# Kernel tuning notes

Measured on AMD Instinct MI355X. Metric: run time of the kernel, lower is better.

Reference implementation:

```python
import jax, jax.numpy as jnp
import numpy as np

D_MODEL = 1024
NHEAD = 16
SPARSITY = 0.9  # keep prob = 1 - sparsity
NEG = -1e30    # stand-in for -inf; avoids NaN on (rare) fully-masked rows
EPS = 1e-5


def _layernorm(x, g, b):
    mu = jnp.mean(x, axis=-1, keepdims=True)
    var = jnp.mean(jnp.square(x - mu), axis=-1, keepdims=True)
    return (x - mu) * jax.lax.rsqrt(var + EPS) * g + b


def setup_inputs() -> dict:
    key = jax.random.key(0)
    ks = jax.random.split(key, 12)
    B, S, D = 2, 2048, D_MODEL
    H = NHEAD
    s = 1.0 / np.sqrt(D)
    inp = {
        "x": jax.random.normal(ks[0], (B, S, D), jnp.float32),
        # torch: torch.rand((B,H,S,S)) > sparsity, resampled each forward
        "mask": jax.random.uniform(ks[1], (B, H, S, S), jnp.float32) > SPARSITY,
        "Wq": jax.random.normal(ks[2], (D, D), jnp.float32) * s,
        "bq": jnp.zeros((D,), jnp.float32),
        "Wk": jax.random.normal(ks[3], (D, D), jnp.float32) * s,
        "bk": jnp.zeros((D,), jnp.float32),
        "Wv": jax.random.normal(ks[4], (D, D), jnp.float32) * s,
        "bv": jnp.zeros((D,), jnp.float32),
        "Wo": jax.random.normal(ks[5], (D, D), jnp.float32) * s,
        "bo": jnp.zeros((D,), jnp.float32),
        "ln1_g": jnp.ones((D,), jnp.float32),
        "ln1_b": jnp.zeros((D,), jnp.float32),
        "ln2_g": jnp.ones((D,), jnp.float32),
        "ln2_b": jnp.zeros((D,), jnp.float32),
        "W1": jax.random.normal(ks[6], (D, 4 * D), jnp.float32) * s,
        "b1f": jnp.zeros((4 * D,), jnp.float32),
        "W2": jax.random.normal(ks[7], (4 * D, D), jnp.float32) * (1.0 / np.sqrt(4 * D)),
        "b2f": jnp.zeros((D,), jnp.float32),
    }
    return inp


def reference(x, mask, Wq, bq, Wk, bk, Wv, bv, Wo, bo,
              ln1_g, ln1_b, ln2_g, ln2_b, W1, b1f, W2, b2f):
    B, S, D = x.shape
    H = NHEAD
    dk = D // H
    # projections -> (B, H, S, dk)
    q = (x @ Wq + bq).reshape(B, S, H, dk).transpose(0, 2, 1, 3)
    k = (x @ Wk + bk).reshape(B, S, H, dk).transpose(0, 2, 1, 3)
    v = (x @ Wv + bv).reshape(B, S, H, dk).transpose(0, 2, 1, 3)
    scores = jnp.einsum('bhqd,bhkd->bhqk', q, k) / np.sqrt(dk)
    scores = jnp.where(mask, scores, NEG)
    attn = jax.nn.softmax(scores, axis=-1)
    ctx = jnp.einsum('bhqk,bhkd->bhqd', attn, v)          # (B,H,S,dk)
    ctx = ctx.transpose(0, 2, 1, 3).reshape(B, S, D)
    attn_out = ctx @ Wo + bo
    x = _layernorm(x + attn_out, ln1_g, ln1_b)
    ff = jax.nn.relu(x @ W1 + b1f) @ W2 + b2f             # eval: dropout off
    return _layernorm(x + ff, ln2_g, ln2_b)
```

## Files before the change

kernel.cpp:

```cpp
#include <hip/hip_runtime.h>
#include <stdint.h>


typedef __attribute__((ext_vector_type(8))) short short8;
typedef __attribute__((ext_vector_type(4))) float f32x4;
typedef __attribute__((ext_vector_type(4))) unsigned short u16x4;

__device__ __forceinline__ unsigned short f2bf(float f) {
    union { float f; unsigned u; } v; v.f = f;
    unsigned r = v.u + 0x7fffu + ((v.u >> 16) & 1u);
    return (unsigned short)(r >> 16);
}

__device__ __forceinline__ void gload16(const void* gsrc, void* ldst) {
    __builtin_amdgcn_global_load_lds(
        (const __attribute__((address_space(1))) void*)gsrc,
        (__attribute__((address_space(3))) void*)ldst,
        16, 0, 0);
}

__device__ __forceinline__ int SWZ(int b) { return b ^ (((b >> 9) & 1) << 5); }

__global__ __launch_bounds__(256) void f32_to_bf16_k(
    const float* __restrict__ in, unsigned short* __restrict__ out, int n4)
{
    int i = blockIdx.x * 256 + threadIdx.x;
    if (i < n4) {
        f32x4 v = *(const f32x4*)&in[(size_t)i * 4];
        u16x4 o = { f2bf(v[0]), f2bf(v[1]), f2bf(v[2]), f2bf(v[3]) };
        *(u16x4*)&out[(size_t)i * 4] = o;
    }
}

__global__ __launch_bounds__(256) void transpose_k(
    const float* __restrict__ W, unsigned short* __restrict__ Wt, int K, int N)
{
    __shared__ float tile[32][33];
    const int n0 = blockIdx.x * 32, k0 = blockIdx.y * 32;
    const int tx = threadIdx.x & 31, ty = threadIdx.x >> 5;
#pragma unroll
    for (int i = 0; i < 32; i += 8)
        tile[ty + i][tx] = W[(size_t)(k0 + ty + i) * N + n0 + tx];
    __syncthreads();
#pragma unroll
    for (int i = 0; i < 32; i += 8)
        Wt[(size_t)(n0 + ty + i) * K + k0 + tx] = f2bf(tile[tx][ty + i]);
}

__global__ __launch_bounds__(256) void vtrans_k(
    const unsigned short* __restrict__ qkv, unsigned short* __restrict__ vt)
{
    __shared__ unsigned short tile[32][34];
    const int s0 = blockIdx.x * 32;
    const int d0 = blockIdx.y * 32;
    const int bh = blockIdx.z, b = bh >> 4, h = bh & 15;
    const int tx = threadIdx.x & 31, ty = threadIdx.x >> 5;
#pragma unroll
    for (int i = 0; i < 32; i += 8)
        tile[ty + i][tx] = qkv[(size_t)(b * 2048 + s0 + ty + i) * 3072 + 2048 + h * 64 + d0 + tx];
    __syncthreads();
#pragma unroll
    for (int i = 0; i < 32; i += 8)
        vt[((size_t)bh * 64 + d0 + ty + i) * 2048 + s0 + tx] = tile[tx][ty + i];
}

__global__ void concat3_k(const float* a, const float* b, const float* c, float* out)
{
    int i = blockIdx.x * 256 + threadIdx.x;
    if (i < 3072) out[i] = (i < 1024) ? a[i] : (i < 2048 ? b[i - 1024] : c[i - 2048]);
}

__global__ __launch_bounds__(1024) void detect_mask_k(
    const unsigned int* __restrict__ m, int* __restrict__ flag)
{
    __shared__ int f1, f2;
    if (threadIdx.x == 0) { f1 = 0; f2 = 0; }
    __syncthreads();
    int l1 = 0, l2 = 0;
    for (int i = threadIdx.x; i < 65536; i += 1024) {
        unsigned v = m[i];
        l1 |= (v > 1u);
        l2 |= (v != 0u && v != 0x3f800000u);
    }
    if (l1) atomicOr(&f1, 1);
    if (l2) atomicOr(&f2, 1);
    __syncthreads();
    if (threadIdx.x == 0) {
        int mode = 0;
        if (f1) mode = f2 ? 1 : 2;
        *flag = mode;
    }
}

__global__ __launch_bounds__(256) void pack_mask_k(
    const void* __restrict__ mask, const int* __restrict__ flag,
    unsigned long long* __restrict__ packed, long long nelem)
{
    const int mode = *flag;
    const long long stride = (long long)gridDim.x * 256;
    long long i = (long long)blockIdx.x * 256 + threadIdx.x;
    if (mode == 0) {
        const int* m = (const int*)mask;
        for (; i < nelem; i += stride) {
            unsigned long long bl = __ballot(m[i] != 0);
            if ((threadIdx.x & 63) == 0) packed[i >> 6] = bl;
        }
    } else if (mode == 1) {
        const unsigned char* m = (const unsigned char*)mask;
        for (; i < nelem; i += stride) {
            unsigned long long bl = __ballot(m[i] != 0);
            if ((threadIdx.x & 63) == 0) packed[i >> 6] = bl;
        }
    } else {
        const float* m = (const float*)mask;
        for (; i < nelem; i += stride) {
            unsigned long long bl = __ballot(m[i] != 0.f);
            if ((threadIdx.x & 63) == 0) packed[i >> 6] = bl;
        }
    }
}

template<int EPI>
__global__ __launch_bounds__(512) void gemm256_bt(
    const unsigned short* __restrict__ A, const unsigned short* __restrict__ Bt,
    const float* __restrict__ bias, void* __restrict__ Cout,
    int M, int N, int K)
{
    __shared__ __align__(16) unsigned short lds[2][2][256 * 64];
    const int t = threadIdx.x;
    const int lane = t & 63;
    const int wid = t >> 6;
    const int l16 = lane & 15, g = lane >> 4;
    const int wr = wid >> 2, wc = wid & 3;

    const int nbx = gridDim.x, nwg = nbx * gridDim.y;
    const int orig = blockIdx.y * nbx + blockIdx.x;
    const int qq = nwg >> 3, rr = nwg & 7;
    const int xcd = orig & 7, idx = orig >> 3;
    const int wg = (xcd < rr) ? (xcd * (qq + 1) + idx)
                              : (rr * (qq + 1) + (xcd - rr) * qq + idx);
    const int bm = (wg / nbx) * 256, bn = (wg % nbx) * 256;

    const int ntiles = K >> 6;
    auto kof = [&](int s) { return (s < ntiles ? s : ntiles - 1) << 6; };

    auto stage_half = [&](const unsigned short* __restrict__ P, int grow0, int k0,
                          int buf, int ab, int half) {
#pragma unroll
        for (int rnd = 0; rnd < 2; ++rnd) {
            const int off = rnd * 8192 + t * 16;
            const int sw  = SWZ(off);
            const int row = off >> 7;
            const int col = (sw & 127) >> 1;
            gload16(&P[(size_t)(grow0 + half * 128 + row) * K + k0 + col],
                    &lds[buf][ab][half * 8192 + (off >> 1)]);
        }
    };

    auto lda = [&](int buf, int m, int kc) -> short8 {
        const int byte = ((m * 32 + wr * 16 + l16) * 64 + kc * 32 + g * 8) * 2;
        return *(const short8*)((const char*)&lds[buf][0][0] + SWZ(byte));
    };
    auto ldb = [&](int buf, int n, int kc) -> short8 {
        const int byte = ((n * 64 + wc * 16 + l16) * 64 + kc * 32 + g * 8) * 2;
        return *(const short8*)((const char*)&lds[buf][1][0] + SWZ(byte));
    };

    f32x4 acc[8][4] = {};
    short8 af[4][2];

    stage_half(A,  bm, 0,  0, 0, 0);
    stage_half(A,  bm, 0,  0, 0, 1);
    stage_half(Bt, bn, 0,  0, 1, 0);
    stage_half(Bt, bn, 0,  0, 1, 1);
    stage_half(A,  bm, 64, 1, 0, 0);
    stage_half(Bt, bn, 64, 1, 1, 0);
    asm volatile("s_waitcnt vmcnt(4)" ::: "memory");
    __builtin_amdgcn_s_barrier();

#define PH(buf, mh, nh, doLoadA, STAGE_STMT, doVM)                                  \
  {                                                                                  \
    if (doLoadA) {                                                                   \
      _Pragma("unroll") for (int mm = 0; mm < 4; ++mm)                               \
      _Pragma("unroll") for (int kc = 0; kc < 2; ++kc)                               \
        af[mm][kc] = lda(buf, (mh) * 4 + mm, kc);                                    \
    }                                                                                \
    short8 bf[2][2];                                                                 \
    _Pragma("unroll") for (int nn = 0; nn < 2; ++nn)                                 \
    _Pragma("unroll") for (int kc = 0; kc < 2; ++kc)                                 \
      bf[nn][kc] = ldb(buf, (nh) * 2 + nn, kc);                                      \
    STAGE_STMT;                                                                      \
    __builtin_amdgcn_s_barrier();                                                    \
    __builtin_amdgcn_s_setprio(1);                                                   \
    _Pragma("unroll") for (int mm = 0; mm < 4; ++mm)                                 \
    _Pragma("unroll") for (int nn = 0; nn < 2; ++nn)                                 \
    _Pragma("unroll") for (int kc = 0; kc < 2; ++kc)                                 \
      acc[(mh) * 4 + mm][(nh) * 2 + nn] = __builtin_amdgcn_mfma_f32_16x16x32_bf16(   \
          af[mm][kc], bf[nn][kc], acc[(mh) * 4 + mm][(nh) * 2 + nn], 0, 0, 0);       \
    __builtin_amdgcn_s_setprio(0);                                                   \
    if (doVM) { asm volatile("s_waitcnt vmcnt(4)" ::: "memory"); }                   \
    __builtin_amdgcn_s_barrier();                                                    \
  }

    const int half_ntiles = ntiles >> 1;
    for (int i = 0; i < half_ntiles; ++i) {
        const int k1 = (2 * i + 1) << 6;
        const int k2 = kof(2 * i + 2);
        const int k3 = kof(2 * i + 3);
        PH(0, 0, 0, 1, (stage_half(A,  bm, k1, 1, 0, 1)), 0)
        PH(0, 0, 1, 0, (stage_half(Bt, bn, k1, 1, 1, 1)), 0)
        PH(0, 1, 0, 1, (stage_half(A,  bm, k2, 0, 0, 0)), 0)
        PH(0, 1, 1, 0, (stage_half(Bt, bn, k2, 0, 1, 0)), 1)
        PH(1, 0, 0, 1, (stage_half(A,  bm, k2, 0, 0, 1)), 0)
        PH(1, 0, 1, 0, (stage_half(Bt, bn, k2, 0, 1, 1)), 0)
        PH(1, 1, 0, 1, (stage_half(A,  bm, k3, 1, 0, 0)), 0)
        PH(1, 1, 1, 0, (stage_half(Bt, bn, k3, 1, 1, 0)), 1)
    }
#undef PH

#pragma unroll
    for (int m = 0; m < 8; ++m) {
        const int row0 = bm + m * 32 + wr * 16 + g * 4;
#pragma unroll
        for (int n = 0; n < 4; ++n) {
            const int col = bn + n * 64 + wc * 16 + l16;
            const float bb = bias[col];
#pragma unroll
            for (int r = 0; r < 4; ++r) {
                float v = acc[m][n][r] + bb;
                if (EPI == 1) v = fmaxf(v, 0.f);
                ((unsigned short*)Cout)[(size_t)(row0 + r) * N + col] = f2bf(v);
            }
        }
    }
}

template<int EPI>
__global__ __launch_bounds__(256) void gemm_bt(
    const unsigned short* __restrict__ A, const unsigned short* __restrict__ Bt,
    const float* __restrict__ bias, const float* __restrict__ resid,
    void* __restrict__ Cout, int M, int N, int K)
{
    __shared__ unsigned short As[128 * 64];
    __shared__ unsigned short Bs[128 * 64];
    const int t = threadIdx.x;
    const int lane = t & 63, wid = t >> 6;
    const int l16 = lane & 15, g = lane >> 4;
    const int wr = wid >> 1, wc = wid & 1;
    const int bm = blockIdx.y * 128, bn = blockIdx.x * 128;

    f32x4 acc[4][4] = {};

    for (int k0 = 0; k0 < K; k0 += 64) {
        __syncthreads();
#pragma unroll
        for (int i = 0; i < 4; ++i) {
            int linear = i * 2048 + t * 8;
            int row = linear >> 6, col = linear & 63;
            gload16(&A[(size_t)(bm + row) * K + k0 + col], &As[linear]);
        }
#pragma unroll
        for (int i = 0; i < 4; ++i) {
            int linear = i * 2048 + t * 8;
            int row = linear >> 6, col = linear & 63;
            gload16(&Bt[(size_t)(bn + row) * K + k0 + col], &Bs[linear]);
        }
        __syncthreads();
#pragma unroll
        for (int kc = 0; kc < 2; ++kc) {
            short8 a[4], b[4];
#pragma unroll
            for (int m = 0; m < 4; ++m)
                a[m] = *(const short8*)&As[(wr * 64 + m * 16 + l16) * 64 + kc * 32 + g * 8];
#pragma unroll
            for (int n = 0; n < 4; ++n)
                b[n] = *(const short8*)&Bs[(wc * 64 + n * 16 + l16) * 64 + kc * 32 + g * 8];
#pragma unroll
            for (int m = 0; m < 4; ++m)
#pragma unroll
                for (int n = 0; n < 4; ++n)
                    acc[m][n] = __builtin_amdgcn_mfma_f32_16x16x32_bf16(a[m], b[n], acc[m][n], 0, 0, 0);
        }
    }

#pragma unroll
    for (int m = 0; m < 4; ++m) {
        const int row0 = bm + wr * 64 + m * 16 + g * 4;
#pragma unroll
        for (int n = 0; n < 4; ++n) {
            const int col = bn + wc * 64 + n * 16 + l16;
            const float bb = bias[col];
#pragma unroll
            for (int r = 0; r < 4; ++r) {
                float v = acc[m][n][r] + bb;
                const size_t idx = (size_t)(row0 + r) * N + col;
                if (EPI == 2) {
                    ((float*)Cout)[idx] = v + resid[idx];
                } else {
                    if (EPI == 1) v = fmaxf(v, 0.f);
                    ((unsigned short*)Cout)[idx] = f2bf(v);
                }
            }
        }
    }
}

__global__ __launch_bounds__(256) void attn_k(
    const unsigned short* __restrict__ qkv,
    const unsigned short* __restrict__ vt,
    const unsigned long long* __restrict__ pmask,
    unsigned short* __restrict__ ctx)
{
    __shared__ unsigned short Pl[4][16 * 72];
    const int t = threadIdx.x, lane = t & 63, w = t >> 6;
    const int l16 = lane & 15, g = lane >> 4;
    const int bh = blockIdx.y;
    const int b = bh >> 4, h = bh & 15;
    const int q0 = blockIdx.x * 64;

    const size_t rowQ = (size_t)(b * 2048 + q0 + w * 16 + l16) * 3072 + h * 64;
    const short8 qf0 = *(const short8*)&qkv[rowQ + g * 8];
    const short8 qf1 = *(const short8*)&qkv[rowQ + 32 + g * 8];

    const unsigned long long* mbase =
        pmask + ((size_t)bh * 2048 + q0 + w * 16 + g * 4) * 32;
    const unsigned short* vbase = &vt[(size_t)bh * 64 * 2048];

    f32x4 acc[4] = {};
    float mrow[4], lrow[4];
#pragma unroll
    for (int j = 0; j < 4; ++j) { mrow[j] = -INFINITY; lrow[j] = 0.f; }

    for (int kt = 0; kt < 32; ++kt) {
        unsigned long long mw[4];
#pragma unroll
        for (int j = 0; j < 4; ++j) mw[j] = mbase[j * 32 + kt];

        f32x4 s[4] = {};
#pragma unroll
        for (int n = 0; n < 4; ++n) {
            const size_t rowK = (size_t)(b * 2048 + kt * 64 + n * 16 + l16) * 3072 + 1024 + h * 64;
            const short8 kf0 = *(const short8*)&qkv[rowK + g * 8];
            const short8 kf1 = *(const short8*)&qkv[rowK + 32 + g * 8];
            s[n] = __builtin_amdgcn_mfma_f32_16x16x32_bf16(qf0, kf0, s[n], 0, 0, 0);
            s[n] = __builtin_amdgcn_mfma_f32_16x16x32_bf16(qf1, kf1, s[n], 0, 0, 0);
        }

#pragma unroll
        for (int n = 0; n < 4; ++n) {
            const int sh = n * 16 + l16;
#pragma unroll
            for (int j = 0; j < 4; ++j) {
                const bool keep = (mw[j] >> sh) & 1ull;
                s[n][j] = keep ? s[n][j] * 0.125f : -1e30f;
            }
        }

#pragma unroll
        for (int j = 0; j < 4; ++j) {
            float mx = fmaxf(fmaxf(s[0][j], s[1][j]), fmaxf(s[2][j], s[3][j]));
#pragma unroll
            for (int d = 1; d < 16; d <<= 1) mx = fmaxf(mx, __shfl_xor(mx, d));
            const float mn = fmaxf(mrow[j], mx);
            float p0 = __expf(s[0][j] - mn), p1 = __expf(s[1][j] - mn);
            float p2 = __expf(s[2][j] - mn), p3 = __expf(s[3][j] - mn);
            s[0][j] = p0; s[1][j] = p1; s[2][j] = p2; s[3][j] = p3;
            float sm = p0 + p1 + p2 + p3;
#pragma unroll
            for (int d = 1; d < 16; d <<= 1) sm += __shfl_xor(sm, d);
            const float scale = __expf(mrow[j] - mn);
            lrow[j] = lrow[j] * scale + sm;
            mrow[j] = mn;
#pragma unroll
            for (int n = 0; n < 4; ++n) acc[n][j] *= scale;
        }

#pragma unroll
        for (int n = 0; n < 4; ++n)
#pragma unroll
            for (int j = 0; j < 4; ++j)
                Pl[w][(g * 4 + j) * 72 + n * 16 + l16] = f2bf(s[n][j]);

#pragma unroll
        for (int c = 0; c < 2; ++c) {
            const short8 pf = *(const short8*)&Pl[w][l16 * 72 + c * 32 + g * 8];
#pragma unroll
            for (int n = 0; n < 4; ++n) {
                const short8 vf = *(const short8*)&vbase[(size_t)(n * 16 + l16) * 2048 + kt * 64 + c * 32 + g * 8];
                acc[n] = __builtin_amdgcn_mfma_f32_16x16x32_bf16(pf, vf, acc[n], 0, 0, 0);
            }
        }
    }

#pragma unroll
    for (int n = 0; n < 4; ++n)
#pragma unroll
        for (int j = 0; j < 4; ++j) {
            const int q = q0 + w * 16 + g * 4 + j;
            ctx[(size_t)(b * 2048 + q) * 1024 + h * 64 + n * 16 + l16] = f2bf(acc[n][j] / lrow[j]);
        }
}

template<int WB>
__global__ __launch_bounds__(256) void ln_k(
    const float* __restrict__ in, const float* __restrict__ gw, const float* __restrict__ bw,
    float* __restrict__ outF, unsigned short* __restrict__ outB)
{
    __shared__ float red[2][4];
    const int row = blockIdx.x, t = threadIdx.x;
    const f32x4 v = *(const f32x4*)&in[(size_t)row * 1024 + t * 4];
    float s = v[0] + v[1] + v[2] + v[3];
    float ss = v[0] * v[0] + v[1] * v[1] + v[2] * v[2] + v[3] * v[3];
#pragma unroll
    for (int d = 1; d < 64; d <<= 1) { s += __shfl_xor(s, d); ss += __shfl_xor(ss, d); }
    if ((t & 63) == 0) { red[0][t >> 6] = s; red[1][t >> 6] = ss; }
    __syncthreads();
    s = red[0][0] + red[0][1] + red[0][2] + red[0][3];
    ss = red[1][0] + red[1][1] + red[1][2] + red[1][3];
    const float mu = s * (1.f / 1024.f);
    const float var = ss * (1.f / 1024.f) - mu * mu;
    const float rs = rsqrtf(var + 1e-5f);
    f32x4 y;
#pragma unroll
    for (int e = 0; e < 4; ++e)
        y[e] = (v[e] - mu) * rs * gw[t * 4 + e] + bw[t * 4 + e];
    *(f32x4*)&outF[(size_t)row * 1024 + t * 4] = y;
    if (WB) {
        u16x4 o = { f2bf(y[0]), f2bf(y[1]), f2bf(y[2]), f2bf(y[3]) };
        *(u16x4*)&outB[(size_t)row * 1024 + t * 4] = o;
    }
}

extern "C" void kernel_launch(void* const* d_in, const int* in_sizes, int n_in,
                              void* d_out, int out_size, void* d_ws, size_t ws_size,
                              hipStream_t stream)
{
    (void)n_in; (void)out_size; (void)ws_size;
    const float* x   = (const float*)d_in[0];
    const void*  mask = d_in[1];
    const float* Wq  = (const float*)d_in[2];
    const float* bq  = (const float*)d_in[3];
    const float* Wk  = (const float*)d_in[4];
    const float* bk  = (const float*)d_in[5];
    const float* Wv  = (const float*)d_in[6];
    const float* bv  = (const float*)d_in[7];
    const float* Wo  = (const float*)d_in[8];
    const float* bo  = (const float*)d_in[9];
    const float* g1  = (const float*)d_in[10];
    const float* be1 = (const float*)d_in[11];
    const float* g2  = (const float*)d_in[12];
    const float* be2 = (const float*)d_in[13];
    const float* W1  = (const float*)d_in[14];
    const float* b1  = (const float*)d_in[15];
    const float* W2  = (const float*)d_in[16];
    const float* b2  = (const float*)d_in[17];

    const int M = 4096;
    const long long maskN = in_sizes[1];

    char* wsb = (char*)d_ws;
    size_t off = 0;
    auto alloc = [&](size_t bytes) -> char* {
        char* p = wsb + off;
        off += (bytes + 255) & ~(size_t)255;
        return p;
    };
    int*            flag   = (int*)           alloc(256);
    unsigned long long* pm = (unsigned long long*)alloc((size_t)(maskN / 64) * 8);
    unsigned short* xb     = (unsigned short*)alloc((size_t)M * 1024 * 2);
    unsigned short* wqkvT  = (unsigned short*)alloc((size_t)3072 * 1024 * 2);
    unsigned short* woT    = (unsigned short*)alloc((size_t)1024 * 1024 * 2);
    unsigned short* w1T    = (unsigned short*)alloc((size_t)4096 * 1024 * 2);
    unsigned short* w2T    = (unsigned short*)alloc((size_t)1024 * 4096 * 2);
    float*          bqkv   = (float*)         alloc(3072 * 4);
    unsigned short* qkv    = (unsigned short*)alloc((size_t)M * 3072 * 2);
    unsigned short* vtb    = (unsigned short*)alloc((size_t)32 * 64 * 2048 * 2);
    unsigned short* ctxb   = (unsigned short*)alloc((size_t)M * 1024 * 2);
    float*          r1f    = (float*)         alloc((size_t)M * 1024 * 4);
    float*          x1f    = (float*)         alloc((size_t)M * 1024 * 4);
    unsigned short* x1b    = (unsigned short*)alloc((size_t)M * 1024 * 2);
    unsigned short* hb     = (unsigned short*)alloc((size_t)M * 4096 * 2);

    detect_mask_k<<<1, 1024, 0, stream>>>((const unsigned int*)mask, flag);
    pack_mask_k<<<2048, 256, 0, stream>>>(mask, flag, pm, maskN);
    f32_to_bf16_k<<<4096, 256, 0, stream>>>(x, xb, M * 1024 / 4);
    transpose_k<<<dim3(32, 32),  256, 0, stream>>>(Wq, wqkvT,                1024, 1024);
    transpose_k<<<dim3(32, 32),  256, 0, stream>>>(Wk, wqkvT + 1024 * 1024,  1024, 1024);
    transpose_k<<<dim3(32, 32),  256, 0, stream>>>(Wv, wqkvT + 2048 * 1024,  1024, 1024);
    transpose_k<<<dim3(32, 32),  256, 0, stream>>>(Wo, woT,                  1024, 1024);
    transpose_k<<<dim3(128, 32), 256, 0, stream>>>(W1, w1T, 1024, 4096);
    transpose_k<<<dim3(32, 128), 256, 0, stream>>>(W2, w2T, 4096, 1024);
    concat3_k<<<12, 256, 0, stream>>>(bq, bk, bv, bqkv);

    gemm256_bt<0><<<dim3(12, 16), 512, 0, stream>>>(xb, wqkvT, bqkv, qkv, M, 3072, 1024);
    vtrans_k<<<dim3(64, 2, 32), 256, 0, stream>>>(qkv, vtb);
    attn_k<<<dim3(32, 32), 256, 0, stream>>>(qkv, vtb, pm, ctxb);
    gemm_bt<2><<<dim3(8, 32), 256, 0, stream>>>(ctxb, woT, bo, x, r1f, M, 1024, 1024);
    ln_k<1><<<4096, 256, 0, stream>>>(r1f, g1, be1, x1f, x1b);
    gemm256_bt<1><<<dim3(16, 16), 512, 0, stream>>>(x1b, w1T, b1, hb, M, 4096, 1024);
    gemm_bt<2><<<dim3(8, 32), 256, 0, stream>>>(hb, w2T, b2, x1f, r1f, M, 1024, 4096);
    ln_k<0><<<4096, 256, 0, stream>>>(r1f, g2, be2, (float*)d_out, nullptr);
}
```

Baseline: 1.295 ms.

## Fuse mask bit-packing into attention kernel and raise MFMA wave priority

Removes the separate pack_mask kernel and its packed-mask buffer. The attention kernel now reads the raw mask directly, building bitmasks per 64-key tile with wave ballots and selecting the rows each lane group needs. It also wraps the MFMA blocks in s_setprio to favour matrix issue. The aim is to avoid one full pass over the large mask plus a launch, at the cost of attention waves loading raw mask bytes inside the inner loop, where that latency may not be hidden.

```diff
diff --git a/kernel.cpp b/kernel.cpp
--- a/kernel.cpp
+++ b/kernel.cpp
@@ -89,34 +89,6 @@
         int mode = 0;
         if (f1) mode = f2 ? 1 : 2;
         *flag = mode;
-    }
-}
-
-__global__ __launch_bounds__(256) void pack_mask_k(
-    const void* __restrict__ mask, const int* __restrict__ flag,
-    unsigned long long* __restrict__ packed, long long nelem)
-{
-    const int mode = *flag;
-    const long long stride = (long long)gridDim.x * 256;
-    long long i = (long long)blockIdx.x * 256 + threadIdx.x;
-    if (mode == 0) {
-        const int* m = (const int*)mask;
-        for (; i < nelem; i += stride) {
-            unsigned long long bl = __ballot(m[i] != 0);
-            if ((threadIdx.x & 63) == 0) packed[i >> 6] = bl;
-        }
-    } else if (mode == 1) {
-        const unsigned char* m = (const unsigned char*)mask;
-        for (; i < nelem; i += stride) {
-            unsigned long long bl = __ballot(m[i] != 0);
-            if ((threadIdx.x & 63) == 0) packed[i >> 6] = bl;
-        }
-    } else {
-        const float* m = (const float*)mask;
-        for (; i < nelem; i += stride) {
-            unsigned long long bl = __ballot(m[i] != 0.f);
-            if ((threadIdx.x & 63) == 0) packed[i >> 6] = bl;
-        }
     }
 }
 
@@ -308,7 +280,8 @@
 __global__ __launch_bounds__(256) void attn_k(
     const unsigned short* __restrict__ qkv,
     const unsigned short* __restrict__ vt,
-    const unsigned long long* __restrict__ pmask,
+    const void* __restrict__ mask,
+    const int* __restrict__ flag,
     unsigned short* __restrict__ ctx)
 {
     __shared__ unsigned short Pl[4][16 * 72];
@@ -317,13 +290,13 @@
     const int bh = blockIdx.y;
     const int b = bh >> 4, h = bh & 15;
     const int q0 = blockIdx.x * 64;
+    const int mode = *flag;
 
     const size_t rowQ = (size_t)(b * 2048 + q0 + w * 16 + l16) * 3072 + h * 64;
     const short8 qf0 = *(const short8*)&qkv[rowQ + g * 8];
     const short8 qf1 = *(const short8*)&qkv[rowQ + 32 + g * 8];
 
-    const unsigned long long* mbase =
-        pmask + ((size_t)bh * 2048 + q0 + w * 16 + g * 4) * 32;
+    const size_t mrow0 = ((size_t)bh * 2048 + q0 + w * 16) * 2048;
     const unsigned short* vbase = &vt[(size_t)bh * 64 * 2048];
 
     f32x4 acc[4] = {};
@@ -332,11 +305,33 @@
     for (int j = 0; j < 4; ++j) { mrow[j] = -INFINITY; lrow[j] = 0.f; }
 
     for (int kt = 0; kt < 32; ++kt) {
+        unsigned long long bl[16];
+        if (mode == 0) {
+            const int* m = (const int*)mask;
+#pragma unroll
+            for (int r = 0; r < 16; ++r)
+                bl[r] = __ballot(m[mrow0 + (size_t)r * 2048 + kt * 64 + lane] != 0);
+        } else if (mode == 1) {
+            const unsigned char* m = (const unsigned char*)mask;
+#pragma unroll
+            for (int r = 0; r < 16; ++r)
+                bl[r] = __ballot(m[mrow0 + (size_t)r * 2048 + kt * 64 + lane] != 0);
+        } else {
+            const float* m = (const float*)mask;
+#pragma unroll
+            for (int r = 0; r < 16; ++r)
+                bl[r] = __ballot(m[mrow0 + (size_t)r * 2048 + kt * 64 + lane] != 0.f);
+        }
         unsigned long long mw[4];
 #pragma unroll
-        for (int j = 0; j < 4; ++j) mw[j] = mbase[j * 32 + kt];
+        for (int j = 0; j < 4; ++j) {
+            const unsigned long long v01 = (g & 1) ? bl[4 + j] : bl[j];
+            const unsigned long long v23 = (g & 1) ? bl[12 + j] : bl[8 + j];
+            mw[j] = (g & 2) ? v23 : v01;
+        }
 
         f32x4 s[4] = {};
+        __builtin_amdgcn_s_setprio(1);
 #pragma unroll
         for (int n = 0; n < 4; ++n) {
             const size_t rowK = (size_t)(b * 2048 + kt * 64 + n * 16 + l16) * 3072 + 1024 + h * 64;
@@ -345,6 +340,7 @@
             s[n] = __builtin_amdgcn_mfma_f32_16x16x32_bf16(qf0, kf0, s[n], 0, 0, 0);
             s[n] = __builtin_amdgcn_mfma_f32_16x16x32_bf16(qf1, kf1, s[n], 0, 0, 0);
         }
+        __builtin_amdgcn_s_setprio(0);
 
 #pragma unroll
         for (int n = 0; n < 4; ++n) {
@@ -381,6 +377,7 @@
             for (int j = 0; j < 4; ++j)
                 Pl[w][(g * 4 + j) * 72 + n * 16 + l16] = f2bf(s[n][j]);
 
+        __builtin_amdgcn_s_setprio(1);
 #pragma unroll
         for (int c = 0; c < 2; ++c) {
             const short8 pf = *(const short8*)&Pl[w][l16 * 72 + c * 32 + g * 8];
@@ -390,6 +387,7 @@
                 acc[n] = __builtin_amdgcn_mfma_f32_16x16x32_bf16(pf, vf, acc[n], 0, 0, 0);
             }
         }
+        __builtin_amdgcn_s_setprio(0);
     }
 
 #pragma unroll
@@ -456,7 +454,6 @@
     const float* b2  = (const float*)d_in[17];
 
     const int M = 4096;
-    const long long maskN = in_sizes[1];
 
     char* wsb = (char*)d_ws;
     size_t off = 0;
@@ -466,7 +463,6 @@
         return p;
     };
     int*            flag   = (int*)           alloc(256);
-    unsigned long long* pm = (unsigned long long*)alloc((size_t)(maskN / 64) * 8);
     unsigned short* xb     = (unsigned short*)alloc((size_t)M * 1024 * 2);
     unsigned short* wqkvT  = (unsigned short*)alloc((size_t)3072 * 1024 * 2);
     unsigned short* woT    = (unsigned short*)alloc((size_t)1024 * 1024 * 2);
@@ -482,7 +478,6 @@
     unsigned short* hb     = (unsigned short*)alloc((size_t)M * 4096 * 2);
 
     detect_mask_k<<<1, 1024, 0, stream>>>((const unsigned int*)mask, flag);
-    pack_mask_k<<<2048, 256, 0, stream>>>(mask, flag, pm, maskN);
     f32_to_bf16_k<<<4096, 256, 0, stream>>>(x, xb, M * 1024 / 4);
     transpose_k<<<dim3(32, 32),  256, 0, stream>>>(Wq, wqkvT,                1024, 1024);
     transpose_k<<<dim3(32, 32),  256, 0, stream>>>(Wk, wqkvT + 1024 * 1024,  1024, 1024);
@@ -494,7 +489,7 @@
 
     gemm256_bt<0><<<dim3(12, 16), 512, 0, stream>>>(xb, wqkvT, bqkv, qkv, M, 3072, 1024);
     vtrans_k<<<dim3(64, 2, 32), 256, 0, stream>>>(qkv, vtb);
-    attn_k<<<dim3(32, 32), 256, 0, stream>>>(qkv, vtb, pm, ctxb);
+    attn_k<<<dim3(32, 32), 256, 0, stream>>>(qkv, vtb, mask, flag, ctxb);
     gemm_bt<2><<<dim3(8, 32), 256, 0, stream>>>(ctxb, woT, bo, x, r1f, M, 1024, 1024);
     ln_k<1><<<4096, 256, 0, stream>>>(r1f, g1, be1, x1f, x1b);
     gemm256_bt<1><<<dim3(16, 16), 512, 0, stream>>>(x1b, w1T, b1, hb, M, 4096, 1024);
```

Result: slower. 1.604 ms (+23.8%).
